# Performance work log

Hardware: AMD Instinct MI355X
Metric: run time of the kernel (lower is better)

Reference implementation:

```python
import jax, jax.numpy as jnp
from jax import lax
import numpy as np

N_SPLITS = 2
N_LEVELS = 3
B, T, C = 32, 1024, 128
HID = 512          # int(input_dim * hidden_size) = 128 * 4
K1, K2 = 5, 3      # first conv kernel_size, second conv kernel=3
N_INTER = 7        # 1 + 2 + 4 interactors in the binary tree
LEAKY_SLOPE = 0.01


def setup_inputs() -> dict:
    key = jax.random.key(0)
    ks = jax.random.split(key, 9)
    w = 0.05  # small init so exp-gating stays well-conditioned
    return {
        "x": jax.random.normal(ks[0], (B, T, C), jnp.float32),
        "mul_w1": jax.random.normal(ks[1], (N_INTER, N_SPLITS, K1, C, HID), jnp.float32) * w,
        "mul_b1": jnp.zeros((N_INTER, N_SPLITS, HID), jnp.float32),
        "mul_w2": jax.random.normal(ks[2], (N_INTER, N_SPLITS, K2, HID, C), jnp.float32) * w,
        "mul_b2": jnp.zeros((N_INTER, N_SPLITS, C), jnp.float32),
        "add_w1": jax.random.normal(ks[3], (N_INTER, N_SPLITS, K1, C, HID), jnp.float32) * w,
        "add_b1": jnp.zeros((N_INTER, N_SPLITS, HID), jnp.float32),
        "add_w2": jax.random.normal(ks[4], (N_INTER, N_SPLITS, K2, HID, C), jnp.float32) * w,
        "add_b2": jnp.zeros((N_INTER, N_SPLITS, C), jnp.float32),
    }


def _leaky(x):
    return jnp.where(x > 0, x, LEAKY_SLOPE * x)


def _causal_conv(x, w, b):
    # x: [B, L, Cin], w: [K, Cin, Cout] (keras WIO layout); 'causal' = left-pad K-1
    k = w.shape[0]
    y = lax.conv_general_dilated(x, w, window_strides=(1,),
                                 padding=[(k - 1, 0)],
                                 dimension_numbers=("NWC", "WIO", "NWC"))
    return y + b


def _conv_seq(x, w1, b1, w2, b2):
    # Conv1D(causal, LeakyReLU 0.01) -> Dropout(identity at inference) -> Conv1D(k=3, causal, tanh)
    h = _leaky(_causal_conv(x, w1, b1))
    return jnp.tanh(_causal_conv(h, w2, b2))


def _interactor(x, idx, p):
    # x: [B, L, C]; strided temporal split into N_SPLITS pieces of length L//N_SPLITS
    splits = [x[:, i::N_SPLITS, :] for i in range(N_SPLITS)]
    scale = N_SPLITS - 1
    mul_list = []
    for i in range(N_SPLITS):
        s = 0.0
        for j in range(N_SPLITS):
            if j != i:
                s = s + _conv_seq(splits[j], p["mul_w1"][idx, i], p["mul_b1"][idx, i],
                                  p["mul_w2"][idx, i], p["mul_b2"][idx, i])
        # prod_j exp(f(x_j)) ** (1/scale) == exp(sum_j f(x_j) / scale)
        mul_list.append(splits[i] * jnp.exp(s / scale))
    out = []
    for i in range(N_SPLITS):
        a = 0.0
        for j in range(N_SPLITS):
            if j != i:
                a = a + _conv_seq(mul_list[j], p["add_w1"][idx, i], p["add_b1"][idx, i],
                                  p["add_w2"][idx, i], p["add_b2"][idx, i])
        a = a / scale
        out.append(mul_list[i] + a if i % 2 == 0 else mul_list[i] - a)
    return out


def reference(x, mul_w1, mul_b1, mul_w2, mul_b2, add_w1, add_b1, add_w2, add_b2):
    p = {"mul_w1": mul_w1, "mul_b1": mul_b1, "mul_w2": mul_w2, "mul_b2": mul_b2,
         "add_w1": add_w1, "add_b1": add_b1, "add_w2": add_w2, "add_b2": add_b2}
    t_in = x.shape[1]
    min_unit = N_SPLITS ** N_LEVELS
    pad = (-t_in) % min_unit  # left zero-pad to a multiple of n_splits**n_levels
    xp = jnp.pad(x, ((0, 0), (pad, 0), (0, 0)))
    seq = [xp]
    idx = 0
    for lvl in range(N_LEVELS):
        nxt = []
        for j in range(N_SPLITS ** lvl):
            nxt += _interactor(seq[j], idx, p)
            idx += 1
        seq = nxt
    # rev_split: recursively concatenate along time with stride `steps`
    while len(seq) > 1:
        steps = len(seq) // N_SPLITS
        seq = [jnp.concatenate([seq[i + s * steps] for s in range(N_SPLITS)], axis=1)
               for i in range(steps)]
    return seq[0][:, -t_in:, :]
```

## Files before the change

kernel.cpp:

```cpp
#include <hip/hip_runtime.h>
#include <hip/hip_bf16.h>
#include <stdint.h>


static constexpr int B_ = 32, T_ = 1024, C_ = 128, HID_ = 512;
static constexpr int K1_ = 5, K2_ = 3;

typedef __attribute__((ext_vector_type(8))) _Float16 half8;
typedef __attribute__((ext_vector_type(4))) float f32x4;

__device__ __forceinline__ unsigned short f2h(float f) {
    _Float16 h = (_Float16)f;
    return __builtin_bit_cast(unsigned short, h);
}

__device__ __forceinline__ void gload16(const void* g, void* l) {
    __builtin_amdgcn_global_load_lds(
        (const __attribute__((address_space(1))) unsigned int*)g,
        (__attribute__((address_space(3))) unsigned int*)l, 16, 0, 0);
}

template<int CIN, int COUT, bool SWZ>
__global__ __launch_bounds__(256)
void wprep_k(const float* __restrict__ win1, unsigned short* __restrict__ wout1,
             const float* __restrict__ win2, unsigned short* __restrict__ wout2,
             int nhalf) {
    constexpr int TA = CIN / 64, TB = COUT / 64;
    int blk = blockIdx.x;
    int tb = blk % TB;
    int ta = (blk / TB) % TA;
    int s  = blk / (TA * TB);
    const float* win;
    unsigned short* wout;
    if (s < nhalf) { win = win1; wout = wout1; }
    else           { win = win2; wout = wout2; s -= nhalf; }
    __shared__ float tile[64][65];
    const float* src = win + (size_t)s * CIN * COUT;
    unsigned short* dst = wout + (size_t)s * CIN * COUT;
    int cl = threadIdx.x & 63;
    int rw = threadIdx.x >> 6;
    for (int r = rw; r < 64; r += 4)
        tile[r][cl] = src[(size_t)(ta * 64 + r) * COUT + tb * 64 + cl];
    __syncthreads();
    for (int r = rw; r < 64; r += 4) {
        int co = tb * 64 + r;
        int ci = ta * 64 + cl;
        int ciw = SWZ ? ((ci & ~127) | ((ci & 127) ^ ((co & 7) << 3))) : ci;
        dst[(size_t)co * CIN + ciw] = f2h(tile[cl][r]);
    }
}

__global__ __launch_bounds__(256)
void split_k(const float* __restrict__ cur, unsigned short* __restrict__ outb,
             int Ls) {
    int idx = blockIdx.x * 256 + threadIdx.x;
    int row = idx >> 5;
    int cq  = (idx & 31) << 2;
    int BLs = B_ * Ls;
    int g  = row / BLs;
    int r2 = row - g * BLs;
    int b  = r2 / Ls;
    int u  = r2 - b * Ls;
    int p = g >> 1, i = g & 1;
    const float4 v = *(const float4*)(cur +
        ((size_t)(p * B_ + b) * (2 * Ls) + 2 * u + i) * C_ + cq);
    ushort4 o;
    o.x = f2h(v.x); o.y = f2h(v.y); o.z = f2h(v.z); o.w = f2h(v.w);
    int cqw = cq ^ (((u + 4) & 7) << 3);
    *(ushort4*)(outb + (size_t)row * C_ + cqw) = o;
}

__global__ __launch_bounds__(256, 2)
void conv1_k(const unsigned short* __restrict__ actb,
             const unsigned short* __restrict__ wL,
             const float* __restrict__ bias,
             unsigned short* __restrict__ hid,
             const unsigned short* __restrict__ zp,
             int Ls, int rsplit, int idxbase) {
    __shared__ unsigned short smemA[2][80 * 128];

    const int tid = threadIdx.x;
    const int lane = tid & 63;
    const int w = tid >> 6;
    const int wr = w >> 1, wc = w & 1;

    const int blk = blockIdx.x;
    const int ct = blk & 7;
    const int rs = (blk >> 3) % rsplit;
    const int g  = (blk >> 3) / rsplit;
    const int n0 = ct * 64;
    const int gin  = g ^ 1;
    const int widx = (idxbase + (g >> 1)) * 2 + (g & 1);

    const char* gbase = (const char*)(actb + (size_t)gin * B_ * Ls * C_);
    const float* bptr = bias + (size_t)widx * HID_;

    const unsigned short* wlane = wL + (size_t)widx * (K1_ * HID_ * C_)
        + (size_t)(n0 + wc * 32 + (lane & 15)) * C_ + ((lane >> 4) << 3);
    half8 breg[K1_][2][4];
#pragma unroll
    for (int t = 0; t < K1_; ++t)
#pragma unroll
        for (int n = 0; n < 2; ++n)
#pragma unroll
            for (int ks = 0; ks < 4; ++ks)
                breg[t][n][ks] = *(const half8*)(wlane
                    + ((size_t)t * HID_ + n * 16) * C_ + ks * 32);

    const float bv0 = bptr[n0 + wc * 32 + (lane & 15)];
    const float bv1 = bptr[n0 + wc * 32 + 16 + (lane & 15)];

    const int rtbase = rs * 8;

    auto stage = [&](int rt, int p) {
        const int b  = (rt * 64) / Ls;
        const int t0 = (rt * 64) % Ls;
        const char* inb = gbase + (size_t)b * Ls * 256;
#pragma unroll
        for (int j = 0; j < 5; ++j) {
            int ch = w * 5 + j;
            int q = ch * 1024 + lane * 16;
            int r = q >> 8;
            int cb = q & 255;
            int t = t0 - 4 + r;
            const char* src = (t >= 0) ? inb + (size_t)t * 256 + cb
                                       : (const char*)zp + cb;
            gload16(src, (char*)smemA[p] + ch * 1024);
        }
    };

    stage(rtbase, 0);
    asm volatile("s_waitcnt vmcnt(0)" ::: "memory");
    __syncthreads();

#pragma unroll
    for (int i = 0; i < 8; ++i) {
        const int rt = rtbase + i;
        const int b  = (rt * 64) / Ls;
        const int t0 = (rt * 64) % Ls;
        const int p  = i & 1;

        __syncthreads();
        if (i < 7) stage(rt + 1, p ^ 1);
        if (i > 0) {
            if (i < 7) {
                asm volatile("s_waitcnt vmcnt(21)" ::: "memory");
            } else {
                asm volatile("s_waitcnt vmcnt(16)" ::: "memory");
            }
            __syncthreads();
        }

        f32x4 acc[2][2];
#pragma unroll
        for (int m = 0; m < 2; ++m)
#pragma unroll
            for (int n = 0; n < 2; ++n) acc[m][n] = (f32x4){0.f, 0.f, 0.f, 0.f};

        const unsigned short* sA = smemA[p];
#pragma unroll
        for (int kk = 0; kk < K1_; ++kk) {
#pragma unroll
            for (int ks = 0; ks < 4; ++ks) {
                half8 aF[2];
                const int cole = ks * 32 + ((lane >> 4) << 3);
#pragma unroll
                for (int m = 0; m < 2; ++m) {
                    int ar = kk + wr * 32 + m * 16 + (lane & 15);
                    aF[m] = *(const half8*)(sA + ar * 128 + (cole ^ ((ar & 7) << 3)));
                }
#pragma unroll
                for (int m = 0; m < 2; ++m) {
                    acc[m][0] = __builtin_amdgcn_mfma_f32_16x16x32_f16(
                        aF[m], breg[kk][0][ks], acc[m][0], 0, 0, 0);
                    acc[m][1] = __builtin_amdgcn_mfma_f32_16x16x32_f16(
                        aF[m], breg[kk][1][ks], acc[m][1], 0, 0, 0);
                }
            }
        }

        unsigned short* outp = hid + ((size_t)(g * B_ + b) * Ls + t0) * HID_;
#pragma unroll
        for (int n = 0; n < 2; ++n) {
            const int co = n0 + wc * 32 + n * 16 + (lane & 15);
            const float bv = n ? bv1 : bv0;
#pragma unroll
            for (int m = 0; m < 2; ++m) {
                const int u0 = wr * 32 + m * 16 + ((lane >> 4) << 2);
#pragma unroll
                for (int q = 0; q < 4; ++q) {
                    float v = acc[m][n][q] + bv;
                    v = (v > 0.f) ? v : 0.01f * v;
                    int t = t0 + u0 + q;
                    int cow = (co & ~127) | ((co & 127) ^ (((t + 2) & 7) << 3));
                    outp[(size_t)(u0 + q) * HID_ + cow] = f2h(v);
                }
            }
        }
    }
}

template<int EPI>
__global__ __launch_bounds__(256, 3)
void conv2_k(const unsigned short* __restrict__ hid,
             const unsigned short* __restrict__ wT,
             const float* __restrict__ bias,
             const float* __restrict__ cur,
             float* __restrict__ mulf,
             unsigned short* __restrict__ actb,
             float* __restrict__ nxt,
             unsigned short* __restrict__ actn,
             float* __restrict__ dout,
             const unsigned short* __restrict__ zp,
             int Ls, int RT, int idxbase) {
    __shared__ unsigned short smemA[66 * 128];
    __shared__ unsigned short smemB[128 * 128];

    const int tid = threadIdx.x;
    const int lane = tid & 63;
    const int w = tid >> 6;
    const int wr = w >> 1, wc = w & 1;

    int blk = blockIdx.x;
    const int rt = blk % RT;
    const int g  = blk / RT;
    const int rowstart = rt * 64;
    const int b  = rowstart / Ls;
    const int t0 = rowstart - b * Ls;
    const int widx = (idxbase + (g >> 1)) * 2 + (g & 1);

    const char* inb = (const char*)(hid + (size_t)(g * B_ + b) * Ls * HID_);
    const char* wb  = (const char*)(wT + (size_t)widx * (K2_ * C_ * HID_));
    const float* bptr = bias + (size_t)widx * C_;

    f32x4 acc[2][4];
#pragma unroll
    for (int m = 0; m < 2; ++m)
#pragma unroll
        for (int n = 0; n < 4; ++n) acc[m][n] = (f32x4){0.f, 0.f, 0.f, 0.f};

    for (int ck = 0; ck < 4; ++ck) {
        if (ck) __syncthreads();
        for (int ch = w; ch < 17; ch += 4) {
            int q = ch * 1024 + lane * 16;
            if (q < 16896) {
                int r = q >> 8;
                int cb = q & 255;
                int t = t0 - 2 + r;
                const char* src = (t >= 0)
                    ? inb + (size_t)t * 1024 + ck * 256 + cb
                    : (const char*)zp + cb;
                gload16(src, (char*)smemA + ch * 1024);
            }
        }
        for (int kk = 0; kk < K2_; ++kk) {
            if (kk) __syncthreads();
            const char* wt = wb + (size_t)kk * C_ * HID_ * 2;
            for (int ch = w; ch < 32; ch += 4) {
                int q = ch * 1024 + lane * 16;
                int co = q >> 8;
                int cb = q & 255;
                gload16(wt + (size_t)co * 1024 + ck * 256 + cb,
                        (char*)smemB + ch * 1024);
            }
            asm volatile("s_waitcnt vmcnt(0)" ::: "memory");
            __syncthreads();

#pragma unroll
            for (int ks = 0; ks < 4; ++ks) {
                half8 aF[2], bF[4];
                const int cole = ks * 32 + ((lane >> 4) << 3);
#pragma unroll
                for (int m = 0; m < 2; ++m) {
                    int ar = kk + wr * 32 + m * 16 + (lane & 15);
                    aF[m] = *(const half8*)(smemA + ar * 128 + (cole ^ ((ar & 7) << 3)));
                }
#pragma unroll
                for (int n = 0; n < 4; ++n) {
                    int br = wc * 64 + n * 16 + (lane & 15);
                    bF[n] = *(const half8*)(smemB + br * 128 + (cole ^ ((br & 7) << 3)));
                }
#pragma unroll
                for (int m = 0; m < 2; ++m)
#pragma unroll
                    for (int n = 0; n < 4; ++n)
                        acc[m][n] = __builtin_amdgcn_mfma_f32_16x16x32_f16(
                            aF[m], bF[n], acc[m][n], 0, 0, 0);
            }
        }
    }

    const size_t rowb = (size_t)(g * B_ + b) * Ls + t0;
    const int p_ = g >> 1, i_ = g & 1;
    const int Ls2 = Ls >> 1;
#pragma unroll
    for (int n = 0; n < 4; ++n) {
        int c = wc * 64 + n * 16 + (lane & 15);
        float bv = bptr[c];
#pragma unroll
        for (int m = 0; m < 2; ++m) {
            int u0 = wr * 32 + m * 16 + ((lane >> 4) << 2);
#pragma unroll
            for (int q = 0; q < 4; ++q) {
                float v = acc[m][n][q] + bv;
                float xc = fminf(fmaxf(v, -15.f), 15.f);
                float e2 = __expf(2.f * xc);
                float th = (e2 - 1.f) / (e2 + 1.f);
                size_t ro = rowb + (size_t)(u0 + q);
                int u = t0 + u0 + q;
                if (EPI == 0) {
                    float sv = cur[((size_t)(p_ * B_ + b) * (2 * Ls) + 2 * u + i_) * C_ + c];
                    float mv = sv * __expf(th);
                    mulf[ro * C_ + c] = mv;
                    int cw = c ^ (((u + 4) & 7) << 3);
                    actb[ro * C_ + cw] = f2h(mv);
                } else {
                    float mv = mulf[ro * C_ + c];
                    float val = (i_ == 0) ? (mv + th) : (mv - th);
                    if (EPI == 1) {
                        nxt[ro * C_ + c] = val;
                        int gq = g * 2 + (u & 1);
                        int uq = u >> 1;
                        int cw = c ^ (((uq + 4) & 7) << 3);
                        actn[((size_t)(gq * B_ + b) * Ls2 + uq) * C_ + cw] = f2h(val);
                    } else {
                        int tau = u | (((g >> 2) & 1) << 7) | (((g >> 1) & 1) << 8)
                                    | ((g & 1) << 9);
                        dout[((size_t)b * T_ + tau) * C_ + c] = val;
                    }
                }
            }
        }
    }
}

extern "C" void kernel_launch(void* const* d_in, const int* in_sizes, int n_in,
                              void* d_out, int out_size, void* d_ws, size_t ws_size,
                              hipStream_t stream) {
    const float* x   = (const float*)d_in[0];
    const float* mw1 = (const float*)d_in[1];
    const float* mb1 = (const float*)d_in[2];
    const float* mw2 = (const float*)d_in[3];
    const float* mb2 = (const float*)d_in[4];
    const float* aw1 = (const float*)d_in[5];
    const float* ab1 = (const float*)d_in[6];
    const float* aw2 = (const float*)d_in[7];
    const float* ab2 = (const float*)d_in[8];

    char* ws = (char*)d_ws;
    size_t off = 0;
    auto alloc = [&](size_t sz) {
        char* p = ws + off;
        off += (sz + 255) & ~(size_t)255;
        return p;
    };
    unsigned short* zp   = (unsigned short*)alloc(8192);
    unsigned short* w1m  = (unsigned short*)alloc((size_t)14 * 5 * 512 * 128 * 2);
    unsigned short* w1a  = (unsigned short*)alloc((size_t)14 * 5 * 512 * 128 * 2);
    unsigned short* w2m  = (unsigned short*)alloc((size_t)14 * 3 * 128 * 512 * 2);
    unsigned short* w2a  = (unsigned short*)alloc((size_t)14 * 3 * 128 * 512 * 2);
    float* bufA          = (float*)alloc((size_t)4194304 * 4);
    float* bufB          = (float*)alloc((size_t)4194304 * 4);
    unsigned short* actb = (unsigned short*)alloc((size_t)4194304 * 2);
    unsigned short* hidb = (unsigned short*)alloc((size_t)16777216 * 2);
    float* mulf          = (float*)alloc((size_t)4194304 * 4);
    (void)ws_size; (void)n_in; (void)in_sizes; (void)out_size;

    hipMemsetAsync(zp, 0, 8192, stream);

    wprep_k<128, 512, false><<<2240, 256, 0, stream>>>(mw1, w1m, aw1, w1a, 70);
    wprep_k<512, 128, true ><<<1344, 256, 0, stream>>>(mw2, w2m, aw2, w2a, 42);

    split_k<<<4096, 256, 0, stream>>>(x, actb, 512);

    for (int lvl = 0; lvl < 3; ++lvl) {
        const int P = 1 << lvl;
        const int G = 2 * P;
        const int Ls = (1024 >> lvl) >> 1;
        const int idxbase = P - 1;
        const float* cur = (lvl == 0) ? x : ((lvl == 1) ? bufA : bufB);
        float* nxt = (lvl == 1) ? bufB : bufA;
        const int rsplit = (B_ * Ls / 64) / 8;
        const int RT2 = Ls / 2;

        conv1_k<<<512, 256, 0, stream>>>(actb, w1m, mb1, hidb, zp,
                                         Ls, rsplit, idxbase);
        conv2_k<0><<<G * RT2, 256, 0, stream>>>(hidb, w2m, mb2, cur, mulf,
                                                actb, nullptr, nullptr, nullptr,
                                                zp, Ls, RT2, idxbase);
        conv1_k<<<512, 256, 0, stream>>>(actb, w1a, ab1, hidb, zp,
                                         Ls, rsplit, idxbase);
        if (lvl < 2) {
            conv2_k<1><<<G * RT2, 256, 0, stream>>>(hidb, w2a, ab2, nullptr, mulf,
                                                    nullptr, nxt, actb, nullptr,
                                                    zp, Ls, RT2, idxbase);
        } else {
            conv2_k<2><<<G * RT2, 256, 0, stream>>>(hidb, w2a, ab2, nullptr, mulf,
                                                    nullptr, nullptr, nullptr,
                                                    (float*)d_out,
                                                    zp, Ls, RT2, idxbase);
        }
    }
}
```

Before: 368.7 us.

## Double-buffer conv2 weight tiles and load activations directly into registers

Conv2 no longer stages the hidden activations in LDS. Each lane now loads its A fragments straight from global memory into registers, which lets conv1 drop its XOR swizzle on stores. The weight tiles are double-buffered in LDS, and the next round's B stage and A register loads are issued before the current MFMAs, giving a 12-round software pipeline. This removes the per-ck barriers and the A staging pass, at the cost of more LDS (two 32KB buffers), more registers for two A fragment sets, and lower occupancy (launch bounds drop from 3 to 2 blocks). The direct A global loads are 16-byte strided row reads that may coalesce less well than the previous LDS path.

```diff
diff --git a/kernel.cpp b/kernel.cpp
--- a/kernel.cpp
+++ b/kernel.cpp
@@ -191,9 +191,7 @@
                 for (int q = 0; q < 4; ++q) {
                     float v = acc[m][n][q] + bv;
                     v = (v > 0.f) ? v : 0.01f * v;
-                    int t = t0 + u0 + q;
-                    int cow = (co & ~127) | ((co & 127) ^ (((t + 2) & 7) << 3));
-                    outp[(size_t)(u0 + q) * HID_ + cow] = f2h(v);
+                    outp[(size_t)(u0 + q) * HID_ + co] = f2h(v);
                 }
             }
         }
@@ -201,7 +199,7 @@
 }
 
 template<int EPI>
-__global__ __launch_bounds__(256, 3)
+__global__ __launch_bounds__(256, 2)
 void conv2_k(const unsigned short* __restrict__ hid,
              const unsigned short* __restrict__ wT,
              const float* __restrict__ bias,
@@ -213,8 +211,7 @@
              float* __restrict__ dout,
              const unsigned short* __restrict__ zp,
              int Ls, int RT, int idxbase) {
-    __shared__ unsigned short smemA[66 * 128];
-    __shared__ unsigned short smemB[128 * 128];
+    __shared__ unsigned short smemB[2][128 * 128];
 
     const int tid = threadIdx.x;
     const int lane = tid & 63;
@@ -229,66 +226,89 @@
     const int t0 = rowstart - b * Ls;
     const int widx = (idxbase + (g >> 1)) * 2 + (g & 1);
 
-    const char* inb = (const char*)(hid + (size_t)(g * B_ + b) * Ls * HID_);
     const char* wb  = (const char*)(wT + (size_t)widx * (K2_ * C_ * HID_));
     const float* bptr = bias + (size_t)widx * C_;
 
+    const int hi8 = (lane >> 4) << 3;
+    const unsigned short* arow[K2_][2];
+#pragma unroll
+    for (int kk = 0; kk < K2_; ++kk)
+#pragma unroll
+        for (int m = 0; m < 2; ++m) {
+            int t = t0 - 2 + kk + wr * 32 + m * 16 + (lane & 15);
+            arow[kk][m] = (t >= 0)
+                ? hid + ((size_t)(g * B_ + b) * Ls + t) * HID_ + hi8
+                : zp + hi8;
+        }
+
+    auto stageB = [&](int ck, int kk, int buf) {
+        const char* wt = wb + (size_t)kk * C_ * HID_ * 2;
+#pragma unroll
+        for (int ch0 = 0; ch0 < 8; ++ch0) {
+            int ch = w * 8 + ch0;
+            int q = ch * 1024 + lane * 16;
+            int co = q >> 8;
+            int cb = q & 255;
+            gload16(wt + (size_t)co * 1024 + ck * 256 + cb,
+                    (char*)smemB[buf] + ch * 1024);
+        }
+    };
+    auto loadA = [&](int r, half8 (&a)[2][4]) {
+        const int ck = r / 3, kk = r % 3;
+#pragma unroll
+        for (int m = 0; m < 2; ++m)
+#pragma unroll
+            for (int ks = 0; ks < 4; ++ks)
+                a[m][ks] = *(const half8*)(arow[kk][m] + ck * 128 + ks * 32);
+    };
+
     f32x4 acc[2][4];
 #pragma unroll
     for (int m = 0; m < 2; ++m)
 #pragma unroll
         for (int n = 0; n < 4; ++n) acc[m][n] = (f32x4){0.f, 0.f, 0.f, 0.f};
 
-    for (int ck = 0; ck < 4; ++ck) {
-        if (ck) __syncthreads();
-        for (int ch = w; ch < 17; ch += 4) {
-            int q = ch * 1024 + lane * 16;
-            if (q < 16896) {
-                int r = q >> 8;
-                int cb = q & 255;
-                int t = t0 - 2 + r;
-                const char* src = (t >= 0)
-                    ? inb + (size_t)t * 1024 + ck * 256 + cb
-                    : (const char*)zp + cb;
-                gload16(src, (char*)smemA + ch * 1024);
+    auto compute = [&](int r, half8 (&a)[2][4]) {
+        const unsigned short* sB = smemB[r & 1];
+#pragma unroll
+        for (int ks = 0; ks < 4; ++ks) {
+            half8 bF[4];
+            const int cole = ks * 32 + hi8;
+#pragma unroll
+            for (int n = 0; n < 4; ++n) {
+                int br = wc * 64 + n * 16 + (lane & 15);
+                bF[n] = *(const half8*)(sB + br * 128 + (cole ^ ((br & 7) << 3)));
             }
-        }
-        for (int kk = 0; kk < K2_; ++kk) {
-            if (kk) __syncthreads();
-            const char* wt = wb + (size_t)kk * C_ * HID_ * 2;
-            for (int ch = w; ch < 32; ch += 4) {
-                int q = ch * 1024 + lane * 16;
-                int co = q >> 8;
-                int cb = q & 255;
-                gload16(wt + (size_t)co * 1024 + ck * 256 + cb,
-                        (char*)smemB + ch * 1024);
-            }
+#pragma unroll
+            for (int m = 0; m < 2; ++m)
+#pragma unroll
+                for (int n = 0; n < 4; ++n)
+                    acc[m][n] = __builtin_amdgcn_mfma_f32_16x16x32_f16(
+                        a[m][ks], bF[n], acc[m][n], 0, 0, 0);
+        }
+    };
+
+    half8 aA[2][4], aB[2][4];
+    stageB(0, 0, 0);
+    loadA(0, aA);
+    asm volatile("s_waitcnt vmcnt(0)" ::: "memory");
+    __syncthreads();
+
+    auto round = [&](int r, half8 (&ac)[2][4], half8 (&an)[2][4]) {
+        if (r < 11) {
+            const int rn = r + 1;
+            stageB(rn / 3, rn % 3, rn & 1);
+            loadA(rn, an);
+        }
+        compute(r, ac);
+        if (r < 11) {
             asm volatile("s_waitcnt vmcnt(0)" ::: "memory");
             __syncthreads();
-
-#pragma unroll
-            for (int ks = 0; ks < 4; ++ks) {
-                half8 aF[2], bF[4];
-                const int cole = ks * 32 + ((lane >> 4) << 3);
-#pragma unroll
-                for (int m = 0; m < 2; ++m) {
-                    int ar = kk + wr * 32 + m * 16 + (lane & 15);
-                    aF[m] = *(const half8*)(smemA + ar * 128 + (cole ^ ((ar & 7) << 3)));
-                }
-#pragma unroll
-                for (int n = 0; n < 4; ++n) {
-                    int br = wc * 64 + n * 16 + (lane & 15);
-                    bF[n] = *(const half8*)(smemB + br * 128 + (cole ^ ((br & 7) << 3)));
-                }
-#pragma unroll
-                for (int m = 0; m < 2; ++m)
-#pragma unroll
-                    for (int n = 0; n < 4; ++n)
-                        acc[m][n] = __builtin_amdgcn_mfma_f32_16x16x32_f16(
-                            aF[m], bF[n], acc[m][n], 0, 0, 0);
-            }
-        }
-    }
+        }
+    };
+    round(0, aA, aB);  round(1, aB, aA);  round(2, aA, aB);  round(3, aB, aA);
+    round(4, aA, aB);  round(5, aB, aA);  round(6, aA, aB);  round(7, aB, aA);
+    round(8, aA, aB);  round(9, aB, aA);  round(10, aA, aB); round(11, aB, aA);
 
     const size_t rowb = (size_t)(g * B_ + b) * Ls + t0;
     const int p_ = g >> 1, i_ = g & 1;
```

New measurement: 430.8 us. 16.8% more time.

## Double-buffer conv2 weight tiles and move conv1 barriers after stores

Applied to the files above, without the earlier changes.

conv2 now streams the weight matrix in 64-output-channel halves into a double-buffered LDS array, prefetching the next half while MFMAs run. A-fragments are held in registers across both halves, and the A tile is restaged once per input-channel chunk. conv1 drops its leading barrier and places the wait-plus-raw-barrier after the epilogue stores. The hidden swizzle offset and the A-row padding change from 2 to 4 so they stay consistent with each other. This aims to remove exposed global-load latency and barrier stalls, at the cost of more LDS and more register pressure.

```diff
diff --git a/kernel.cpp b/kernel.cpp
--- a/kernel.cpp
+++ b/kernel.cpp
@@ -19,6 +19,9 @@
         (const __attribute__((address_space(1))) unsigned int*)g,
         (__attribute__((address_space(3))) unsigned int*)l, 16, 0, 0);
 }
+
+#define VMCNT(N) asm volatile("s_waitcnt vmcnt(" #N ")" ::: "memory")
+#define RAWBAR() __builtin_amdgcn_s_barrier()
 
 template<int CIN, int COUT, bool SWZ>
 __global__ __launch_bounds__(256)
@@ -130,8 +133,8 @@
     };
 
     stage(rtbase, 0);
-    asm volatile("s_waitcnt vmcnt(0)" ::: "memory");
-    __syncthreads();
+    VMCNT(0);
+    RAWBAR();
 
 #pragma unroll
     for (int i = 0; i < 8; ++i) {
@@ -140,16 +143,7 @@
         const int t0 = (rt * 64) % Ls;
         const int p  = i & 1;
 
-        __syncthreads();
         if (i < 7) stage(rt + 1, p ^ 1);
-        if (i > 0) {
-            if (i < 7) {
-                asm volatile("s_waitcnt vmcnt(21)" ::: "memory");
-            } else {
-                asm volatile("s_waitcnt vmcnt(16)" ::: "memory");
-            }
-            __syncthreads();
-        }
 
         f32x4 acc[2][2];
 #pragma unroll
@@ -192,10 +186,15 @@
                     float v = acc[m][n][q] + bv;
                     v = (v > 0.f) ? v : 0.01f * v;
                     int t = t0 + u0 + q;
-                    int cow = (co & ~127) | ((co & 127) ^ (((t + 2) & 7) << 3));
+                    int cow = (co & ~127) | ((co & 127) ^ (((t + 4) & 7) << 3));
                     outp[(size_t)(u0 + q) * HID_ + cow] = f2h(v);
                 }
             }
+        }
+
+        if (i < 7) {
+            VMCNT(16);
+            RAWBAR();
         }
     }
 }
@@ -213,13 +212,14 @@
              float* __restrict__ dout,
              const unsigned short* __restrict__ zp,
              int Ls, int RT, int idxbase) {
-    __shared__ unsigned short smemA[66 * 128];
-    __shared__ unsigned short smemB[128 * 128];
+    __shared__ unsigned short smemA[80 * 128];
+    __shared__ unsigned short smemB[2][64 * 128];
 
     const int tid = threadIdx.x;
     const int lane = tid & 63;
     const int w = tid >> 6;
     const int wr = w >> 1, wc = w & 1;
+    const int hi8 = (lane >> 4) << 3;
 
     int blk = blockIdx.x;
     const int rt = blk % RT;
@@ -233,60 +233,91 @@
     const char* wb  = (const char*)(wT + (size_t)widx * (K2_ * C_ * HID_));
     const float* bptr = bias + (size_t)widx * C_;
 
+    const int bco = (lane * 16) >> 8;
+    const int bcb = (lane * 16) & 255;
+
+    auto stageA = [&](int ck) {
+#pragma unroll
+        for (int j = 0; j < 5; ++j) {
+            int ch = w * 5 + j;
+            int q = ch * 1024 + lane * 16;
+            int r = q >> 8;
+            int cb = q & 255;
+            int t = t0 - 4 + r;
+            const char* src = (t >= 0) ? inb + (size_t)t * 1024 + ck * 256 + cb
+                                       : (const char*)zp + cb;
+            gload16(src, (char*)smemA + ch * 1024);
+        }
+    };
+    auto stageB = [&](int p) {
+        const int r = p >> 1, h = p & 1;
+        const int ck = r / 3, kk = r % 3;
+        const char* wt = wb + (size_t)kk * C_ * HID_ * 2;
+#pragma unroll
+        for (int j = 0; j < 4; ++j) {
+            int ch = w * 4 + j;
+            int co = h * 64 + ch * 4 + bco;
+            gload16(wt + (size_t)co * 1024 + ck * 256 + bcb,
+                    (char*)smemB[p & 1] + ch * 1024);
+        }
+    };
+
     f32x4 acc[2][4];
 #pragma unroll
     for (int m = 0; m < 2; ++m)
 #pragma unroll
         for (int n = 0; n < 4; ++n) acc[m][n] = (f32x4){0.f, 0.f, 0.f, 0.f};
 
-    for (int ck = 0; ck < 4; ++ck) {
-        if (ck) __syncthreads();
-        for (int ch = w; ch < 17; ch += 4) {
-            int q = ch * 1024 + lane * 16;
-            if (q < 16896) {
-                int r = q >> 8;
-                int cb = q & 255;
-                int t = t0 - 2 + r;
-                const char* src = (t >= 0)
-                    ? inb + (size_t)t * 1024 + ck * 256 + cb
-                    : (const char*)zp + cb;
-                gload16(src, (char*)smemA + ch * 1024);
+    half8 af[2][4];
+
+    stageA(0);
+    stageB(0);
+    VMCNT(0);
+    RAWBAR();
+
+#pragma unroll
+    for (int p = 0; p < 24; ++p) {
+        const int r = p >> 1, h = p & 1;
+        const int ck = r / 3, kk = r % 3;
+
+        if (p) {
+            VMCNT(0);
+            RAWBAR();
+        }
+        if (p + 1 < 24) stageB(p + 1);
+
+        if (h == 0) {
+#pragma unroll
+            for (int m = 0; m < 2; ++m)
+#pragma unroll
+                for (int ks = 0; ks < 4; ++ks) {
+                    int ar = 2 + kk + wr * 32 + m * 16 + (lane & 15);
+                    af[m][ks] = *(const half8*)(smemA + ar * 128
+                        + ((ks * 32 + hi8) ^ ((ar & 7) << 3)));
+                }
+        }
+
+        const unsigned short* sB = smemB[p & 1];
+#pragma unroll
+        for (int ks = 0; ks < 4; ++ks) {
+            half8 bF[2];
+            const int cole = ks * 32 + hi8;
+#pragma unroll
+            for (int n = 0; n < 2; ++n) {
+                int br = wc * 32 + n * 16 + (lane & 15);
+                bF[n] = *(const half8*)(sB + br * 128 + (cole ^ ((br & 7) << 3)));
             }
-        }
-        for (int kk = 0; kk < K2_; ++kk) {
-            if (kk) __syncthreads();
-            const char* wt = wb + (size_t)kk * C_ * HID_ * 2;
-            for (int ch = w; ch < 32; ch += 4) {
-                int q = ch * 1024 + lane * 16;
-                int co = q >> 8;
-                int cb = q & 255;
-                gload16(wt + (size_t)co * 1024 + ck * 256 + cb,
-                        (char*)smemB + ch * 1024);
-            }
-            asm volatile("s_waitcnt vmcnt(0)" ::: "memory");
-            __syncthreads();
-
-#pragma unroll
-            for (int ks = 0; ks < 4; ++ks) {
-                half8 aF[2], bF[4];
-                const int cole = ks * 32 + ((lane >> 4) << 3);
-#pragma unroll
-                for (int m = 0; m < 2; ++m) {
-                    int ar = kk + wr * 32 + m * 16 + (lane & 15);
-                    aF[m] = *(const half8*)(smemA + ar * 128 + (cole ^ ((ar & 7) << 3)));
-                }
-#pragma unroll
-                for (int n = 0; n < 4; ++n) {
-                    int br = wc * 64 + n * 16 + (lane & 15);
-                    bF[n] = *(const half8*)(smemB + br * 128 + (cole ^ ((br & 7) << 3)));
-                }
-#pragma unroll
-                for (int m = 0; m < 2; ++m)
-#pragma unroll
-                    for (int n = 0; n < 4; ++n)
-                        acc[m][n] = __builtin_amdgcn_mfma_f32_16x16x32_f16(
-                            aF[m], bF[n], acc[m][n], 0, 0, 0);
-            }
+#pragma unroll
+            for (int m = 0; m < 2; ++m)
+#pragma unroll
+                for (int n = 0; n < 2; ++n)
+                    acc[m][h * 2 + n] = __builtin_amdgcn_mfma_f32_16x16x32_f16(
+                        af[m][ks], bF[n], acc[m][h * 2 + n], 0, 0, 0);
+        }
+
+        if ((p % 6 == 5) && p < 23) {
+            RAWBAR();
+            stageA(ck + 1);
         }
     }
 
@@ -294,15 +325,15 @@
     const int p_ = g >> 1, i_ = g & 1;
     const int Ls2 = Ls >> 1;
 #pragma unroll
-    for (int n = 0; n < 4; ++n) {
-        int c = wc * 64 + n * 16 + (lane & 15);
+    for (int nn = 0; nn < 4; ++nn) {
+        int c = (nn >> 1) * 64 + wc * 32 + (nn & 1) * 16 + (lane & 15);
         float bv = bptr[c];
 #pragma unroll
         for (int m = 0; m < 2; ++m) {
             int u0 = wr * 32 + m * 16 + ((lane >> 4) << 2);
 #pragma unroll
             for (int q = 0; q < 4; ++q) {
-                float v = acc[m][n][q] + bv;
+                float v = acc[m][nn][q] + bv;
                 float xc = fminf(fmaxf(v, -15.f), 15.f);
                 float e2 = __expf(2.f * xc);
                 float th = (e2 - 1.f) / (e2 + 1.f);
```

After: 390.5 us. 1.06x slower.
